# Kernel tuning notes

Measured on AMD Instinct MI355X. Metric: run time of the kernel, lower is better.

The kernel has to match this reference:

```python
import jax, jax.numpy as jnp
import numpy as np

B, S, D, H = 4, 2048, 1024, 16
DK = D // H


def setup_inputs() -> dict:
    key = jax.random.key(0)
    ks = jax.random.split(key, 10)
    s = 1.0 / np.sqrt(D)
    return {
        "key": jax.random.normal(ks[0], (B, S, D), jnp.float32),
        "query": jax.random.normal(ks[1], (B, S, D), jnp.float32),
        "value": jax.random.normal(ks[2], (B, S, D), jnp.float32),
        "mask": jax.random.randint(ks[3], (B, S), 0, 2).astype(jnp.bool_),
        "Wq": jax.random.normal(ks[4], (D, D), jnp.float32) * s,
        "bq": jax.random.normal(ks[5], (D,), jnp.float32) * s,
        "Wk": jax.random.normal(ks[6], (D, D), jnp.float32) * s,
        "bk": jax.random.normal(ks[7], (D,), jnp.float32) * s,
        "Wv": jax.random.normal(ks[8], (D, D), jnp.float32) * s,
        "bv": jax.random.normal(ks[9], (D,), jnp.float32) * s,
    }


def reference(key, query, value, mask, Wq, bq, Wk, bk, Wv, bv):
    # Linear projections (torch Linear: x @ W^T + b)
    q = query @ Wq.T + bq  # [B,S,D]
    k = key @ Wk.T + bk
    v = value @ Wv.T + bv
    # split heads -> [B,H,S,dk]
    q = q.reshape(B, S, H, DK).transpose(0, 2, 1, 3)
    k = k.reshape(B, S, H, DK).transpose(0, 2, 1, 3)
    v = v.reshape(B, S, H, DK).transpose(0, 2, 1, 3)
    # non-standard scale: divide by d_model
    scores = jnp.einsum("bhqd,bhkd->bhqk", q, k) / jnp.float32(D)
    att = jax.nn.softmax(scores, axis=-1)
    # mask applied AFTER softmax: masked positions set to 1e-15
    m = mask[:, None, None, :] | mask[:, None, :, None]  # [B,1,S,S]
    att = jnp.where(m, jnp.float32(1e-15), att)
    out = jnp.einsum("bhqk,bhkd->bhqd", att, v)
    return out.transpose(0, 2, 1, 3).reshape(B, S, D)
```

## Files before the change

kernel.cpp:

```cpp
#include <hip/hip_runtime.h>
#include <stdint.h>

#define B_  4
#define S_  2048
#define D_  1024
#define H_  16
#define DK_ 64
#define NX  ((size_t)8388608)
#define NW  ((size_t)1048576)

typedef __bf16 bf16x8 __attribute__((ext_vector_type(8)));
typedef float  f32x4  __attribute__((ext_vector_type(4)));
typedef float  f32x2  __attribute__((ext_vector_type(2)));
typedef unsigned int uint32x2 __attribute__((ext_vector_type(2)));

__device__ __forceinline__ unsigned short bfbits(float f) {
  union { __bf16 h; unsigned short u; } c;
  c.h = (__bf16)f;
  return c.u;
}

__device__ __forceinline__ unsigned int pkbf(float a, float b) {
  union { __bf16 h[2]; unsigned int u; } c;
  c.h[0] = (__bf16)a; c.h[1] = (__bf16)b;
  return c.u;
}

__device__ __forceinline__ f32x2 pk_fma(f32x2 a, f32x2 b, f32x2 c) {
  f32x2 d;
  asm("v_pk_fma_f32 %0, %1, %2, %3" : "=v"(d) : "v"(a), "v"(b), "v"(c));
  return d;
}
__device__ __forceinline__ f32x2 pk_add(f32x2 a, f32x2 b) {
  f32x2 d;
  asm("v_pk_add_f32 %0, %1, %2" : "=v"(d) : "v"(a), "v"(b));
  return d;
}

__device__ __forceinline__ f32x2 exp2_poly2(f32x2 x) {
  const f32x2 c3 = {0.05550411f, 0.05550411f};
  const f32x2 c2 = {0.24022651f, 0.24022651f};
  const f32x2 c1 = {0.69314718f, 0.69314718f};
  const f32x2 one = {1.0f, 1.0f};
  f32x2 t = pk_fma(x, c3, c2);
  t = pk_fma(x, t, c1);
  t = pk_fma(x, t, one);
  return t;
}

__device__ __forceinline__ void async16(const unsigned short* g, unsigned short* l) {
  __builtin_amdgcn_global_load_lds(
      (const __attribute__((address_space(1))) unsigned short*)g,
      (__attribute__((address_space(3))) unsigned short*)l, 16, 0, 0);
}

__global__ void cvt6(const float* __restrict__ s0, const float* __restrict__ s1,
                     const float* __restrict__ s2, const float* __restrict__ s3,
                     const float* __restrict__ s4, const float* __restrict__ s5,
                     const unsigned int* __restrict__ maskw,
                     int* __restrict__ flag,
                     unsigned short* __restrict__ dst) {
  if (blockIdx.x == 0) {
    __shared__ int bad;
    if (threadIdx.x == 0) bad = 0;
    __syncthreads();
    int any = 0;
    for (int i = threadIdx.x; i < 2048; i += 256)
      if (maskw[i] > 1u) any = 1;
    if (any) atomicOr(&bad, 1);
    __syncthreads();
    if (threadIdx.x == 0) *flag = bad;
  }
  size_t i4 = (size_t)blockIdx.x * 256 + threadIdx.x;
  size_t e = i4 * 4;
  const float* src;
  unsigned short* d;
  size_t off;
  if (e < 3 * NX) {
    int which = (int)(e >> 23);
    off = e & (NX - 1);
    src = which == 0 ? s0 : (which == 1 ? s1 : s2);
    d = dst + NX * which;
  } else {
    size_t e2 = e - 3 * NX;
    int which = (int)(e2 >> 20);
    off = e2 & (NW - 1);
    src = which == 0 ? s3 : (which == 1 ? s4 : s5);
    d = dst + 3 * NX + NW * which;
  }
  float4 f = *(const float4*)(src + off);
  ushort4 hv;
  hv.x = bfbits(f.x); hv.y = bfbits(f.y); hv.z = bfbits(f.z); hv.w = bfbits(f.w);
  *(ushort4*)(d + off) = hv;
}

__global__ __launch_bounds__(256) void proj_gemm(
    const unsigned short* __restrict__ Xb, const unsigned short* __restrict__ Wb,
    const float* __restrict__ bqp, const float* __restrict__ bkp,
    const float* __restrict__ bvp, const void* __restrict__ maskp,
    const int* __restrict__ flagp, unsigned short* __restrict__ outb) {
  int id = blockIdx.x;
  int gLow = id & 7, x = (id >> 3) & 7, gHigh = id >> 6;
  int g = gHigh * 8 + gLow;
  int z = g >> 6, y = g & 63;

  const unsigned short* A;
  const unsigned short* Bm;
  int m0, n0;
  if (z == 2) {
    A  = Wb + NW * 2;
    Bm = Xb + NX * 2;
    m0 = x * 128;
    n0 = y * 128;
  } else {
    A  = Xb + NX * z;
    Bm = Wb + NW * z;
    m0 = y * 128;
    n0 = x * 128;
  }
  const float* bias = (z == 0) ? bqp : ((z == 1) ? bkp : bvp);
  unsigned short* dst = outb + NX * z;

  __shared__ unsigned short smem[2 * 128 * 64];
  unsigned short* As = smem;
  unsigned short* Bs = smem + 128 * 64;
  unsigned short* tr = smem;

  int tid = threadIdx.x;
  int wid = tid >> 6, lane = tid & 63;
  int wm = wid >> 1, wn = wid & 1;
  int fr = lane & 15, quad = lane >> 4;
  int sr = lane >> 3, c8 = lane & 7, g8 = c8 ^ sr;

  const f32x4 zero = {0.f, 0.f, 0.f, 0.f};
  f32x4 acc[4][4];
  for (int i = 0; i < 4; ++i)
    for (int j = 0; j < 4; ++j) acc[i][j] = zero;

  for (int kt = 0; kt < 16; ++kt) {
    int k0 = kt * 64;
    __syncthreads();
#pragma unroll
    for (int i = 0; i < 4; ++i) {
      int row = wid * 32 + i * 8 + sr;
      async16(A  + (size_t)(m0 + row) * 1024 + k0 + g8 * 8, &As[row * 64 + c8 * 8]);
      async16(Bm + (size_t)(n0 + row) * 1024 + k0 + g8 * 8, &Bs[row * 64 + c8 * 8]);
    }
    __syncthreads();
#pragma unroll
    for (int kk = 0; kk < 2; ++kk) {
      bf16x8 af[4], bfr[4];
#pragma unroll
      for (int t = 0; t < 4; ++t)
        af[t] = *(const bf16x8*)&As[(wm * 64 + t * 16 + fr) * 64 +
                                    (((kk << 2) | quad) ^ (fr & 7)) * 8];
#pragma unroll
      for (int t = 0; t < 4; ++t)
        bfr[t] = *(const bf16x8*)&Bs[(wn * 64 + t * 16 + fr) * 64 +
                                     (((kk << 2) | quad) ^ (fr & 7)) * 8];
#pragma unroll
      for (int mt = 0; mt < 4; ++mt)
#pragma unroll
        for (int nt = 0; nt < 4; ++nt)
          acc[mt][nt] = __builtin_amdgcn_mfma_f32_16x16x32_bf16(af[mt], bfr[nt],
                                                                acc[mt][nt], 0, 0, 0);
    }
  }

  float scale = (z == 0) ? 0.0014088818758681284f : 1.0f;
  int byteMode = *flagp;
  const unsigned char* m8 = (const unsigned char*)maskp;
  const int* m32 = (const int*)maskp;

  for (int c = 0; c < 2; ++c) {
    __syncthreads();
    if (wm == c) {
#pragma unroll
      for (int nt = 0; nt < 4; ++nt) {
        int ni = n0 + wn * 64 + nt * 16 + fr;
        float badd = 0.f, mmul = 1.f;
        if (z == 2) {
          int bi = ni >> 11, si = ni & 2047;
          int mv = byteMode ? (int)m8[bi * S_ + si] : m32[bi * S_ + si];
          if (mv) mmul = 0.f;
        } else {
          badd = bias[ni];
        }
#pragma unroll
        for (int mt = 0; mt < 4; ++mt) {
          float4 b4;
          if (z == 2) b4 = *(const float4*)&bias[m0 + c * 64 + mt * 16 + quad * 4];
#pragma unroll
          for (int r = 0; r < 4; ++r) {
            float bb = (z == 2) ? ((const float*)&b4)[r] : badd;
            float v = (acc[mt][nt][r] + bb) * scale * mmul;
            int lr = mt * 16 + quad * 4 + r;
            int lc = wn * 64 + nt * 16 + fr;
            tr[lr * 136 + lc] = bfbits(v);
          }
        }
      }
    }
    __syncthreads();
#pragma unroll
    for (int it = 0; it < 4; ++it) {
      int seg = tid + it * 256;
      int row = seg >> 4, s8 = seg & 15;
      uint4 pv = *(const uint4*)&tr[row * 136 + s8 * 8];
      int m = m0 + c * 64 + row;
      int ni0 = n0 + s8 * 8;
      size_t addr;
      if (z == 2) {
        int hh = m >> 6, dc = m & 63;
        int bi = ni0 >> 11, si = ni0 & 2047;
        addr = ((size_t)(bi * 16 + hh) * 64 + dc) * 2048 + si;
      } else {
        int bi = m >> 11, si = m & 2047;
        int hh = ni0 >> 6, dc = ni0 & 63;
        addr = ((size_t)(bi * 16 + hh) * 2048 + si) * 64 + dc;
      }
      *(uint4*)&dst[addr] = pv;
    }
  }
}

__global__ __launch_bounds__(256, 2) void attn4(
    const unsigned short* __restrict__ Qh, const unsigned short* __restrict__ Kh,
    const unsigned short* __restrict__ Vt, const void* __restrict__ maskp,
    const int* __restrict__ flagp, float* __restrict__ out) {
  int id = blockIdx.x;
  int bh = (id >> 7) * 8 + (id & 7);
  int q0 = ((id >> 3) & 15) * 128;
  int b = bh >> 4;
  int tid = threadIdx.x, w = tid >> 6, lane = tid & 63;
  int fr = lane & 15, quad = lane >> 4;
  int wq0 = q0 + w * 32;

  __shared__ unsigned short Ks[128 * 64];
  __shared__ unsigned short Vs[64 * 128];

  int byteMode = *flagp;
  const unsigned char* m8 = (const unsigned char*)maskp;
  const int* m32 = (const int*)maskp;
  float rowm[2];
#pragma unroll
  for (int qt = 0; qt < 2; ++qt) {
    int qi = wq0 + qt * 16 + fr;
    int mv = byteMode ? (int)m8[b * S_ + qi] : m32[b * S_ + qi];
    rowm[qt] = mv ? 0.f : 1.f;
  }

  const unsigned short* Qg = Qh + (size_t)bh * S_ * DK_;
  bf16x8 qf[2][2];
#pragma unroll
  for (int qt = 0; qt < 2; ++qt)
#pragma unroll
    for (int c = 0; c < 2; ++c)
      qf[qt][c] = *(const bf16x8*)&Qg[(size_t)(wq0 + qt * 16 + fr) * 64 + c * 32 + quad * 8];

  const f32x4 zero = {0.f, 0.f, 0.f, 0.f};
  f32x4 accO[4][2];
#pragma unroll
  for (int i = 0; i < 4; ++i)
#pragma unroll
    for (int j = 0; j < 2; ++j) accO[i][j] = zero;
  f32x2 den2[2] = {{0.f, 0.f}, {0.f, 0.f}};

  const unsigned short* Kg = Kh + (size_t)bh * S_ * DK_;
  const unsigned short* Vg = Vt + (size_t)bh * DK_ * S_;

  int krow0 = w * 32 + (lane >> 3);
  int kc8 = lane & 7;
  int vrow0 = w * 16 + (lane >> 4);
  int vc16 = lane & 15;

  for (int kt = 0; kt < 16; ++kt) {
    int k0 = kt * 128;
    __syncthreads();
#pragma unroll
    for (int i = 0; i < 4; ++i) {
      int kr = krow0 + i * 8;
      int kg8 = kc8 ^ (kr & 7);
      async16(Kg + (size_t)(k0 + kr) * 64 + kg8 * 8, &Ks[kr * 64 + kc8 * 8]);
      int vr = vrow0 + i * 4;
      int vg = vc16 ^ (vr & 7);
      async16(Vg + (size_t)vr * S_ + k0 + vg * 8, &Vs[vr * 128 + vc16 * 8]);
    }
    __syncthreads();

#pragma unroll
    for (int kci = 0; kci < 4; ++kci) {
      int kc = (kci + w) & 3;
      bf16x8 kf[2][2];
#pragma unroll
      for (int t2 = 0; t2 < 2; ++t2) {
        int row = kc * 32 + t2 * 16 + fr;
#pragma unroll
        for (int c = 0; c < 2; ++c)
          kf[t2][c] = *(const bf16x8*)&Ks[row * 64 + ((c * 4 + quad) ^ (fr & 7)) * 8];
      }
      f32x4 s2[2][2];
      __builtin_amdgcn_s_setprio(1);
#pragma unroll
      for (int t2 = 0; t2 < 2; ++t2)
#pragma unroll
        for (int qt = 0; qt < 2; ++qt) {
          f32x4 a = __builtin_amdgcn_mfma_f32_16x16x32_bf16(kf[t2][0], qf[qt][0], zero, 0, 0, 0);
          s2[t2][qt] = __builtin_amdgcn_mfma_f32_16x16x32_bf16(kf[t2][1], qf[qt][1], a, 0, 0, 0);
        }
      __builtin_amdgcn_s_setprio(0);
      bf16x8 pvf[2];
#pragma unroll
      for (int qt = 0; qt < 2; ++qt) {
        f32x2 pa0 = {s2[0][qt][0], s2[0][qt][1]};
        f32x2 pa1 = {s2[0][qt][2], s2[0][qt][3]};
        f32x2 pb0 = {s2[1][qt][0], s2[1][qt][1]};
        f32x2 pb1 = {s2[1][qt][2], s2[1][qt][3]};
        pa0 = exp2_poly2(pa0);
        pa1 = exp2_poly2(pa1);
        pb0 = exp2_poly2(pb0);
        pb1 = exp2_poly2(pb1);
        den2[qt] = pk_add(den2[qt], pk_add(pk_add(pa0, pa1), pk_add(pb0, pb1)));
        unsigned int pk00 = pkbf(pa0.x, pa0.y);
        unsigned int pk01 = pkbf(pa1.x, pa1.y);
        unsigned int pk10 = pkbf(pb0.x, pb0.y);
        unsigned int pk11 = pkbf(pb1.x, pb1.y);
        uint32x2 t;
        t = __builtin_amdgcn_permlane32_swap(pk00, pk10, false, false); pk00 = t.x; pk10 = t.y;
        t = __builtin_amdgcn_permlane32_swap(pk01, pk11, false, false); pk01 = t.x; pk11 = t.y;
        t = __builtin_amdgcn_permlane16_swap(pk00, pk10, false, false); pk00 = t.x; pk10 = t.y;
        t = __builtin_amdgcn_permlane16_swap(pk01, pk11, false, false); pk01 = t.x; pk11 = t.y;
        union { unsigned int u[4]; bf16x8 v; } pun;
        pun.u[0] = pk00; pun.u[1] = pk01; pun.u[2] = pk10; pun.u[3] = pk11;
        pvf[qt] = pun.v;
      }
      bf16x8 vf[4];
#pragma unroll
      for (int dt = 0; dt < 4; ++dt)
        vf[dt] = *(const bf16x8*)&Vs[(dt * 16 + fr) * 128 +
                                     ((kc * 4 + quad) ^ (fr & 7)) * 8];
      __builtin_amdgcn_s_setprio(1);
#pragma unroll
      for (int qt = 0; qt < 2; ++qt)
#pragma unroll
        for (int dt = 0; dt < 4; ++dt)
          accO[dt][qt] = __builtin_amdgcn_mfma_f32_16x16x32_bf16(vf[dt], pvf[qt],
                                                                 accO[dt][qt], 0, 0, 0);
      __builtin_amdgcn_s_setprio(0);
    }
  }

  int hcol = (bh & 15) * DK_;
#pragma unroll
  for (int qt = 0; qt < 2; ++qt) {
    float d = den2[qt].x + den2[qt].y;
    d += __shfl_xor(d, 16);
    d += __shfl_xor(d, 32);
    float rinv = rowm[qt] / d;
    int qi = wq0 + qt * 16 + fr;
#pragma unroll
    for (int dt = 0; dt < 4; ++dt) {
      float4 o;
      o.x = accO[dt][qt][0] * rinv;
      o.y = accO[dt][qt][1] * rinv;
      o.z = accO[dt][qt][2] * rinv;
      o.w = accO[dt][qt][3] * rinv;
      int dc = hcol + dt * 16 + quad * 4;
      *(float4*)&out[((size_t)b * S_ + qi) * D_ + dc] = o;
    }
  }
}

extern "C" void kernel_launch(void* const* d_in, const int* in_sizes, int n_in,
                              void* d_out, int out_size, void* d_ws, size_t ws_size,
                              hipStream_t stream) {
  const float* key   = (const float*)d_in[0];
  const float* query = (const float*)d_in[1];
  const float* value = (const float*)d_in[2];
  const void*  mask  = d_in[3];
  const float* Wq    = (const float*)d_in[4];
  const float* bq    = (const float*)d_in[5];
  const float* Wk    = (const float*)d_in[6];
  const float* bk    = (const float*)d_in[7];
  const float* Wv    = (const float*)d_in[8];
  const float* bv    = (const float*)d_in[9];

  unsigned short* ws  = (unsigned short*)d_ws;
  unsigned short* Xb  = ws;
  unsigned short* Wb  = ws + 3 * NX;
  unsigned short* QKV = Wb + 3 * NW;
  int* flag = (int*)(QKV + 3 * NX);
  float* out = (float*)d_out;

  cvt6<<<dim3(27648), dim3(256), 0, stream>>>(query, key, value, Wq, Wk, Wv,
                                              (const unsigned int*)mask, flag, ws);

  proj_gemm<<<dim3(1536), dim3(256), 0, stream>>>(Xb, Wb, bq, bk, bv, mask, flag, QKV);

  attn4<<<dim3(1024), dim3(256), 0, stream>>>(QKV, QKV + NX, QKV + 2 * NX,
                                              mask, flag, out);
}
```

Measured before the change: 315.6 us.

## Load K and V fragments directly from global memory, dropping LDS staging

The attention kernel no longer stages K and V tiles into shared memory with async copies and two barriers per tile. Each wave now reads its MFMA fragments for K and V straight from global memory, relying on L1/L2 caching across the four waves that share a block. This removes the LDS round trip and the synchronisation, but each wave now issues its own redundant global loads, and these loads have higher latency with nothing prefetching them ahead of use.

```diff
diff --git a/kernel.cpp b/kernel.cpp
--- a/kernel.cpp
+++ b/kernel.cpp
@@ -236,9 +236,6 @@
   int fr = lane & 15, quad = lane >> 4;
   int wq0 = q0 + w * 32;
 
-  __shared__ unsigned short Ks[128 * 64];
-  __shared__ unsigned short Vs[64 * 128];
-
   int byteMode = *flagp;
   const unsigned char* m8 = (const unsigned char*)maskp;
   const int* m32 = (const int*)maskp;
@@ -266,39 +263,28 @@
     for (int j = 0; j < 2; ++j) accO[i][j] = zero;
   f32x2 den2[2] = {{0.f, 0.f}, {0.f, 0.f}};
 
-  const unsigned short* Kg = Kh + (size_t)bh * S_ * DK_;
-  const unsigned short* Vg = Vt + (size_t)bh * DK_ * S_;
-
-  int krow0 = w * 32 + (lane >> 3);
-  int kc8 = lane & 7;
-  int vrow0 = w * 16 + (lane >> 4);
-  int vc16 = lane & 15;
-
+  const unsigned short* Kbase = Kh + (size_t)bh * S_ * DK_ +
+                                (size_t)fr * 64 + quad * 8;
+  const unsigned short* Vbase = Vt + (size_t)bh * DK_ * S_ +
+                                (size_t)fr * S_ + quad * 8;
+
+#pragma unroll 1
   for (int kt = 0; kt < 16; ++kt) {
     int k0 = kt * 128;
-    __syncthreads();
-#pragma unroll
-    for (int i = 0; i < 4; ++i) {
-      int kr = krow0 + i * 8;
-      int kg8 = kc8 ^ (kr & 7);
-      async16(Kg + (size_t)(k0 + kr) * 64 + kg8 * 8, &Ks[kr * 64 + kc8 * 8]);
-      int vr = vrow0 + i * 4;
-      int vg = vc16 ^ (vr & 7);
-      async16(Vg + (size_t)vr * S_ + k0 + vg * 8, &Vs[vr * 128 + vc16 * 8]);
-    }
-    __syncthreads();
-
-#pragma unroll
-    for (int kci = 0; kci < 4; ++kci) {
-      int kc = (kci + w) & 3;
+#pragma unroll
+    for (int kc = 0; kc < 4; ++kc) {
+      int kr = k0 + kc * 32;
       bf16x8 kf[2][2];
 #pragma unroll
-      for (int t2 = 0; t2 < 2; ++t2) {
-        int row = kc * 32 + t2 * 16 + fr;
+      for (int t2 = 0; t2 < 2; ++t2)
 #pragma unroll
         for (int c = 0; c < 2; ++c)
-          kf[t2][c] = *(const bf16x8*)&Ks[row * 64 + ((c * 4 + quad) ^ (fr & 7)) * 8];
-      }
+          kf[t2][c] = *(const bf16x8*)&Kbase[(size_t)(kr + t2 * 16) * 64 + c * 32];
+      bf16x8 vf[4];
+#pragma unroll
+      for (int dt = 0; dt < 4; ++dt)
+        vf[dt] = *(const bf16x8*)&Vbase[(size_t)(dt * 16) * S_ + kr];
+
       f32x4 s2[2][2];
       __builtin_amdgcn_s_setprio(1);
 #pragma unroll
@@ -334,11 +320,6 @@
         pun.u[0] = pk00; pun.u[1] = pk01; pun.u[2] = pk10; pun.u[3] = pk11;
         pvf[qt] = pun.v;
       }
-      bf16x8 vf[4];
-#pragma unroll
-      for (int dt = 0; dt < 4; ++dt)
-        vf[dt] = *(const bf16x8*)&Vs[(dt * 16 + fr) * 128 +
-                                     ((kc * 4 + quad) ^ (fr & 7)) * 8];
       __builtin_amdgcn_s_setprio(1);
 #pragma unroll
       for (int qt = 0; qt < 2; ++qt)
```

Result: slower. 455.5 us (+44.3%).
